# Kernel tuning notes

Hardware: AMD Instinct MI355X
Metric: run time of the kernel (lower is better)

The kernel has to match this reference:

```python
import jax, jax.numpy as jnp
import numpy as np

N, L2, C = 4096, 49, 128   # lmax=6 -> (lmax+1)**2 = 49
RES = 18                   # grid resolution (beta, alpha)


def setup_inputs() -> dict:
    key = jax.random.key(0)
    k1, k2, k3 = jax.random.split(key, 3)
    inputs = jax.random.normal(k1, (N, L2, C), dtype=jnp.float32)
    # Stand-ins for the precomputed spherical-harmonic transform matrices
    # (to_grid_mat / from_grid_mat), shape (res_beta, res_alpha, (lmax+1)**2).
    W_to = jax.random.normal(k2, (RES, RES, L2), dtype=jnp.float32) / jnp.sqrt(jnp.float32(L2))
    W_from = jax.random.normal(k3, (RES, RES, L2), dtype=jnp.float32) / jnp.sqrt(jnp.float32(RES * RES))
    return {"inputs": inputs, "W_to": W_to, "W_from": W_from}


def reference(inputs, W_to, W_from):
    # to_grid: coefficients -> real-space S2 grid  (n, beta, alpha, c)
    grid = jnp.einsum('bai,nic->nbac', W_to, inputs)
    # elementwise self tensor product on the grid
    grid = grid * grid
    # from_grid: project back to spherical-harmonic coefficients (n, i, c)
    outputs = jnp.einsum('bai,nbac->nic', W_from, grid)
    return outputs
```

## Files before the change

kernel.cpp:

```cpp
#include <hip/hip_runtime.h>


#define NN    4096
#define L2D   49
#define CCH   128
#define GTOT  324
#define MT1P  22
#define KC2   11

typedef __attribute__((ext_vector_type(8))) short bf16x8;
typedef __attribute__((ext_vector_type(4))) float f32x4;

#define WT_SHORTS (MT1P * 2 * 64 * 8)
#define WF_SHORTS (4 * KC2 * 64 * 8)

__device__ __forceinline__ short f2bf(float f) {
    union { float f; unsigned u; } x; x.f = f;
    return (short)((x.u + 0x7fffu + ((x.u >> 16) & 1u)) >> 16);
}

__global__ void prep_w_kernel(const float* __restrict__ Wt,
                              const float* __restrict__ Wf,
                              short* __restrict__ WtF,
                              short* __restrict__ WfF)
{
    int idx = blockIdx.x * 256 + threadIdx.x;
    if (idx < WT_SHORTS) {
        int j = idx & 7, lane = (idx >> 3) & 63, kcx = (idx >> 9) & 1, mt = idx >> 10;
        int g = mt * 16 + (lane & 15);
        int i = kcx * 32 + (lane >> 4) * 8 + j;
        WtF[idx] = f2bf((g < GTOT && i < L2D) ? Wt[g * L2D + i] : 0.0f);
    } else if (idx < WT_SHORTS + WF_SHORTS) {
        int e = idx - WT_SHORTS;
        int j = e & 7, lane = (e >> 3) & 63, t = e >> 9;
        int kc2 = t % KC2, it = t / KC2;
        int i = it * 16 + (lane & 15);
        int g = kc2 * 32 + (j >> 2) * 16 + (lane >> 4) * 4 + (j & 3);
        WfF[e] = f2bf((g < GTOT && i < L2D) ? Wf[g * L2D + i] : 0.0f);
    }
}

__global__ __launch_bounds__(256, 3)
void stp_mfma2_kernel(const float* __restrict__ inp,
                      const short* __restrict__ WtF,
                      const short* __restrict__ WfF,
                      float* __restrict__ out)
{
    const int tid  = threadIdx.x;
    const int lane = tid & 63;
    const int wave = tid >> 6;
    const int lm   = lane & 15;
    const int quad = lane >> 4;

    const int task = blockIdx.x * 4 + wave;
    const int n    = task >> 1;
    const int h    = task & 1;

    const float* __restrict__ Xn = inp + (size_t)n * (L2D * CCH);

    bf16x8 Bx[4][2];
    #pragma unroll
    for (int t = 0; t < 4; ++t) {
        const int c = h * 64 + t * 16 + lm;
        #pragma unroll
        for (int kcx = 0; kcx < 2; ++kcx) {
            bf16x8 b;
            #pragma unroll
            for (int j = 0; j < 8; ++j) {
                const int i = kcx * 32 + quad * 8 + j;
                float v = 0.0f;
                if (i < L2D) v = Xn[i * CCH + c];
                b[j] = f2bf(v);
            }
            Bx[t][kcx] = b;
        }
    }

    f32x4 acc2[4][4];
    #pragma unroll
    for (int it = 0; it < 4; ++it)
        #pragma unroll
        for (int t = 0; t < 4; ++t)
            acc2[it][t] = (f32x4){0.0f, 0.0f, 0.0f, 0.0f};

    #pragma unroll 1
    for (int kc2 = 0; kc2 < KC2; ++kc2) {
        bf16x8 Wtf[2][2];
        #pragma unroll
        for (int tt = 0; tt < 2; ++tt)
            #pragma unroll
            for (int kcx = 0; kcx < 2; ++kcx)
                Wtf[tt][kcx] = *(const bf16x8*)&WtF[(((2 * kc2 + tt) * 2 + kcx) * 64 + lane) * 8];
        bf16x8 Wff[4];
        #pragma unroll
        for (int it = 0; it < 4; ++it)
            Wff[it] = *(const bf16x8*)&WfF[((it * KC2 + kc2) * 64 + lane) * 8];

        #pragma unroll
        for (int t = 0; t < 4; ++t) {
            bf16x8 Bg;
            #pragma unroll
            for (int tt = 0; tt < 2; ++tt) {
                f32x4 gacc = (f32x4){0.0f, 0.0f, 0.0f, 0.0f};
                gacc = __builtin_amdgcn_mfma_f32_16x16x32_bf16(Wtf[tt][0], Bx[t][0], gacc, 0, 0, 0);
                gacc = __builtin_amdgcn_mfma_f32_16x16x32_bf16(Wtf[tt][1], Bx[t][1], gacc, 0, 0, 0);
                #pragma unroll
                for (int r = 0; r < 4; ++r)
                    Bg[tt * 4 + r] = f2bf(gacc[r] * gacc[r]);
            }
            #pragma unroll
            for (int it = 0; it < 4; ++it)
                acc2[it][t] = __builtin_amdgcn_mfma_f32_16x16x32_bf16(Wff[it], Bg, acc2[it][t], 0, 0, 0);
        }
    }

    float* __restrict__ On = out + (size_t)n * (L2D * CCH);
    #pragma unroll
    for (int it = 0; it < 4; ++it) {
        #pragma unroll
        for (int t = 0; t < 4; ++t) {
            const int c = h * 64 + t * 16 + lm;
            #pragma unroll
            for (int r = 0; r < 4; ++r) {
                const int i = it * 16 + quad * 4 + r;
                if (i < L2D) On[i * CCH + c] = acc2[it][t][r];
            }
        }
    }
}

extern "C" void kernel_launch(void* const* d_in, const int* in_sizes, int n_in,
                              void* d_out, int out_size, void* d_ws, size_t ws_size,
                              hipStream_t stream) {
    const float* inp = (const float*)d_in[0];
    const float* Wt  = (const float*)d_in[1];
    const float* Wf  = (const float*)d_in[2];
    float* out = (float*)d_out;

    short* WtF = (short*)d_ws;
    short* WfF = WtF + WT_SHORTS;

    const int prep_threads = WT_SHORTS + WF_SHORTS;
    prep_w_kernel<<<(prep_threads + 255) / 256, 256, 0, stream>>>(Wt, Wf, WtF, WfF);
    stp_mfma2_kernel<<<2048, 256, 0, stream>>>(inp, WtF, WfF, out);
}
```

Baseline: 214.3 us.

## Process two samples per wave to amortize weight fragment loads

Each wave now handles two batch samples instead of one, so the per-iteration loads of the to-grid and from-grid weight fragments are reused across both samples, and the grid is halved to 1024 blocks. Float-to-bf16 conversion uses a packed two-value intrinsic in place of the manual rounding code, and output stores are made nontemporal. Accumulator and input registers double, so launch bounds drop to 2 blocks per CU, which lowers occupancy and may hurt latency hiding.

```diff
diff --git a/kernel.cpp b/kernel.cpp
--- a/kernel.cpp
+++ b/kernel.cpp
@@ -1,4 +1,5 @@
 #include <hip/hip_runtime.h>
+#include <hip/hip_bf16.h>
 
 
 #define NN    4096
@@ -17,6 +18,12 @@
 __device__ __forceinline__ short f2bf(float f) {
     union { float f; unsigned u; } x; x.f = f;
     return (short)((x.u + 0x7fffu + ((x.u >> 16) & 1u)) >> 16);
+}
+
+__device__ __forceinline__ unsigned pack2bf(float a, float b) {
+    __hip_bfloat162 p = __float22bfloat162_rn(make_float2(a, b));
+    union { __hip_bfloat162 h; unsigned u; } c; c.h = p;
+    return c.u;
 }
 
 __global__ void prep_w_kernel(const float* __restrict__ Wt,
@@ -40,8 +47,8 @@
     }
 }
 
-__global__ __launch_bounds__(256, 3)
-void stp_mfma2_kernel(const float* __restrict__ inp,
+__global__ __launch_bounds__(256, 2)
+void stp_mfma3_kernel(const float* __restrict__ inp,
                       const short* __restrict__ WtF,
                       const short* __restrict__ WfF,
                       float* __restrict__ out)
@@ -53,35 +60,40 @@
     const int quad = lane >> 4;
 
     const int task = blockIdx.x * 4 + wave;
-    const int n    = task >> 1;
+    const int np   = task >> 1;
     const int h    = task & 1;
+    const int n0   = np * 2;
 
-    const float* __restrict__ Xn = inp + (size_t)n * (L2D * CCH);
-
-    bf16x8 Bx[4][2];
+    bf16x8 Bx[2][4][2];
     #pragma unroll
-    for (int t = 0; t < 4; ++t) {
-        const int c = h * 64 + t * 16 + lm;
+    for (int nn = 0; nn < 2; ++nn) {
+        const float* __restrict__ Xn = inp + (size_t)(n0 + nn) * (L2D * CCH);
         #pragma unroll
-        for (int kcx = 0; kcx < 2; ++kcx) {
-            bf16x8 b;
+        for (int t = 0; t < 4; ++t) {
+            const int c = h * 64 + t * 16 + lm;
             #pragma unroll
-            for (int j = 0; j < 8; ++j) {
-                const int i = kcx * 32 + quad * 8 + j;
-                float v = 0.0f;
-                if (i < L2D) v = Xn[i * CCH + c];
-                b[j] = f2bf(v);
+            for (int kcx = 0; kcx < 2; ++kcx) {
+                union { bf16x8 v; unsigned u[4]; } pk;
+                #pragma unroll
+                for (int d = 0; d < 4; ++d) {
+                    const int i0 = kcx * 32 + quad * 8 + 2 * d;
+                    float a = (i0     < L2D) ? Xn[(i0    ) * CCH + c] : 0.0f;
+                    float b = (i0 + 1 < L2D) ? Xn[(i0 + 1) * CCH + c] : 0.0f;
+                    pk.u[d] = pack2bf(a, b);
+                }
+                Bx[nn][t][kcx] = pk.v;
             }
-            Bx[t][kcx] = b;
         }
     }
 
-    f32x4 acc2[4][4];
+    f32x4 acc2[2][4][4];
     #pragma unroll
-    for (int it = 0; it < 4; ++it)
+    for (int nn = 0; nn < 2; ++nn)
         #pragma unroll
-        for (int t = 0; t < 4; ++t)
-            acc2[it][t] = (f32x4){0.0f, 0.0f, 0.0f, 0.0f};
+        for (int it = 0; it < 4; ++it)
+            #pragma unroll
+            for (int t = 0; t < 4; ++t)
+                acc2[nn][it][t] = (f32x4){0.0f, 0.0f, 0.0f, 0.0f};
 
     #pragma unroll 1
     for (int kc2 = 0; kc2 < KC2; ++kc2) {
@@ -97,33 +109,38 @@
             Wff[it] = *(const bf16x8*)&WfF[((it * KC2 + kc2) * 64 + lane) * 8];
 
         #pragma unroll
-        for (int t = 0; t < 4; ++t) {
-            bf16x8 Bg;
+        for (int nn = 0; nn < 2; ++nn) {
             #pragma unroll
-            for (int tt = 0; tt < 2; ++tt) {
-                f32x4 gacc = (f32x4){0.0f, 0.0f, 0.0f, 0.0f};
-                gacc = __builtin_amdgcn_mfma_f32_16x16x32_bf16(Wtf[tt][0], Bx[t][0], gacc, 0, 0, 0);
-                gacc = __builtin_amdgcn_mfma_f32_16x16x32_bf16(Wtf[tt][1], Bx[t][1], gacc, 0, 0, 0);
+            for (int t = 0; t < 4; ++t) {
+                union { bf16x8 v; unsigned u[4]; } bg;
                 #pragma unroll
-                for (int r = 0; r < 4; ++r)
-                    Bg[tt * 4 + r] = f2bf(gacc[r] * gacc[r]);
+                for (int tt = 0; tt < 2; ++tt) {
+                    f32x4 g = (f32x4){0.0f, 0.0f, 0.0f, 0.0f};
+                    g = __builtin_amdgcn_mfma_f32_16x16x32_bf16(Wtf[tt][0], Bx[nn][t][0], g, 0, 0, 0);
+                    g = __builtin_amdgcn_mfma_f32_16x16x32_bf16(Wtf[tt][1], Bx[nn][t][1], g, 0, 0, 0);
+                    bg.u[tt * 2 + 0] = pack2bf(g[0] * g[0], g[1] * g[1]);
+                    bg.u[tt * 2 + 1] = pack2bf(g[2] * g[2], g[3] * g[3]);
+                }
+                #pragma unroll
+                for (int it = 0; it < 4; ++it)
+                    acc2[nn][it][t] = __builtin_amdgcn_mfma_f32_16x16x32_bf16(Wff[it], bg.v, acc2[nn][it][t], 0, 0, 0);
             }
-            #pragma unroll
-            for (int it = 0; it < 4; ++it)
-                acc2[it][t] = __builtin_amdgcn_mfma_f32_16x16x32_bf16(Wff[it], Bg, acc2[it][t], 0, 0, 0);
         }
     }
 
-    float* __restrict__ On = out + (size_t)n * (L2D * CCH);
     #pragma unroll
-    for (int it = 0; it < 4; ++it) {
+    for (int nn = 0; nn < 2; ++nn) {
+        float* __restrict__ On = out + (size_t)(n0 + nn) * (L2D * CCH);
         #pragma unroll
-        for (int t = 0; t < 4; ++t) {
-            const int c = h * 64 + t * 16 + lm;
+        for (int it = 0; it < 4; ++it) {
             #pragma unroll
-            for (int r = 0; r < 4; ++r) {
-                const int i = it * 16 + quad * 4 + r;
-                if (i < L2D) On[i * CCH + c] = acc2[it][t][r];
+            for (int t = 0; t < 4; ++t) {
+                const int c = h * 64 + t * 16 + lm;
+                #pragma unroll
+                for (int r = 0; r < 4; ++r) {
+                    const int i = it * 16 + quad * 4 + r;
+                    if (i < L2D) __builtin_nontemporal_store(acc2[nn][it][t][r], &On[i * CCH + c]);
+                }
             }
         }
     }
@@ -142,5 +159,5 @@
 
     const int prep_threads = WT_SHORTS + WF_SHORTS;
     prep_w_kernel<<<(prep_threads + 255) / 256, 256, 0, stream>>>(Wt, Wf, WtF, WfF);
-    stp_mfma2_kernel<<<2048, 256, 0, stream>>>(inp, WtF, WfF, out);
+    stp_mfma3_kernel<<<1024, 256, 0, stream>>>(inp, WtF, WfF, out);
 }
```

Result: slower. 242.1 us (+13.0%).
